# Kernel optimization log

Measured on AMD Instinct MI355X. Metric: run time of the kernel, lower is better.

Reference implementation:

```python
import jax, jax.numpy as jnp
import numpy as np

B, S, R, H = 16, 2048, 196, 768


def setup_inputs() -> dict:
    key = jax.random.key(0)
    ks = jax.random.split(key, 7)
    sc = 1.0 / np.sqrt(H)
    return {
        "text_features": jax.random.normal(ks[0], (B, S, H), jnp.float32),
        "img_features": jax.random.normal(ks[1], (B, R, H), jnp.float32),
        "W_text": jax.random.normal(ks[2], (H, H), jnp.float32) * sc,
        "b_text": jax.random.normal(ks[3], (H,), jnp.float32) * sc,
        "W_img": jax.random.normal(ks[4], (H, H), jnp.float32) * sc,
        "w_att": jax.random.normal(ks[5], (2 * H,), jnp.float32) * sc,
        "b_att": jax.random.normal(ks[6], (1,), jnp.float32) * sc,
    }


def reference(text_features, img_features, W_text, b_text, W_img, w_att, b_att):
    # Original: repeat text over regions, repeat img over seq, project, concat,
    # tanh, score via att_linear, softmax over regions, weighted sum of img.
    # tanh(concat(t, i)) = concat(tanh(t), tanh(i)), and the concat linear
    # splits into two dot products, so we avoid materializing (B,S,R,2H).
    H_ = text_features.shape[-1]
    t = jnp.tanh(jnp.einsum('bsh,oh->bso', text_features, W_text) + b_text)  # (B,S,H)
    i = jnp.tanh(jnp.einsum('brh,oh->bro', img_features, W_img))             # (B,R,H)
    w1, w2 = w_att[:H_], w_att[H_:]
    # score[b,s,r] = t[b,s]@w1 + i[b,r]@w2 + b_att
    scores = (t @ w1)[:, :, None] + (i @ w2)[:, None, :] + b_att[0]          # (B,S,R)
    att = jax.nn.softmax(scores, axis=-1)
    # weighted sum over regions of the ORIGINAL img features
    return jnp.einsum('bsr,brh->bsh', att, img_features)                      # (B,S,H)
```

## Files before the change

kernel.cpp:

```cpp
#include <hip/hip_runtime.h>
#include <math.h>

#define Bb   16
#define Ss   2048
#define Rr   196
#define Hh   768
#define Mtot (Bb * Rr)
#define NT   (Hh / 64)
#define LDA  72

typedef __attribute__((ext_vector_type(8))) short short8;
typedef __attribute__((ext_vector_type(4))) short short4v;
typedef __attribute__((ext_vector_type(4))) float f32x4;

__device__ inline short f2bf(float f) {
    unsigned u = __builtin_bit_cast(unsigned, f);
    u += 0x7fff + ((u >> 16) & 1);
    return (short)(u >> 16);
}

__global__ __launch_bounds__(256) void k0_cvt(
    const f32x4* __restrict__ a, short4v* __restrict__ da, int na4,
    const f32x4* __restrict__ b, short4v* __restrict__ db)
{
    int gid = blockIdx.x * 256 + threadIdx.x;
    const f32x4* s;
    short4v* d;
    int i;
    if (gid < na4) { s = a; d = da; i = gid; }
    else           { s = b; d = db; i = gid - na4; }
    f32x4 x = s[i];
    short4v o;
    o.x = f2bf(x.x); o.y = f2bf(x.y); o.z = f2bf(x.z); o.w = f2bf(x.w);
    d[i] = o;
}

template <bool FROM_F32>
__global__ __launch_bounds__(256) void k1_mfma(
    const void* __restrict__ Ap, const void* __restrict__ Bp,
    const float* __restrict__ w_att, float* __restrict__ part)
{
    const int m0   = blockIdx.x * 64;
    const int n0   = blockIdx.y * 64;
    const int t    = threadIdx.x;
    const int lane = t & 63;
    const int wv   = t >> 6;
    const int wm   = (wv & 1) * 32;
    const int wn   = (wv >> 1) * 32;
    const int col  = lane & 15;
    const int quad = lane >> 4;

    __shared__ short As[64 * LDA];
    __shared__ short Bs[64 * LDA];
    __shared__ float red[64][2];

    f32x4 acc[2][2] = {};

    const int sm = t >> 2;
    const int sq = t & 3;

    for (int k0 = 0; k0 < Hh; k0 += 64) {
        short8 areg[2], breg[2];
        if (FROM_F32) {
            const float* A = (const float*)Ap;
            const float* B = (const float*)Bp;
#pragma unroll
            for (int j = 0; j < 2; ++j) {
                float4 lo = *(const float4*)&A[(size_t)(m0 + sm) * Hh + k0 + sq * 16 + j * 8];
                float4 hi = *(const float4*)&A[(size_t)(m0 + sm) * Hh + k0 + sq * 16 + j * 8 + 4];
                areg[j][0] = f2bf(lo.x); areg[j][1] = f2bf(lo.y);
                areg[j][2] = f2bf(lo.z); areg[j][3] = f2bf(lo.w);
                areg[j][4] = f2bf(hi.x); areg[j][5] = f2bf(hi.y);
                areg[j][6] = f2bf(hi.z); areg[j][7] = f2bf(hi.w);
                lo = *(const float4*)&B[(size_t)(n0 + sm) * Hh + k0 + sq * 16 + j * 8];
                hi = *(const float4*)&B[(size_t)(n0 + sm) * Hh + k0 + sq * 16 + j * 8 + 4];
                breg[j][0] = f2bf(lo.x); breg[j][1] = f2bf(lo.y);
                breg[j][2] = f2bf(lo.z); breg[j][3] = f2bf(lo.w);
                breg[j][4] = f2bf(hi.x); breg[j][5] = f2bf(hi.y);
                breg[j][6] = f2bf(hi.z); breg[j][7] = f2bf(hi.w);
            }
        } else {
            const short* A = (const short*)Ap;
            const short* B = (const short*)Bp;
#pragma unroll
            for (int j = 0; j < 2; ++j) {
                areg[j] = *(const short8*)&A[(size_t)(m0 + sm) * Hh + k0 + sq * 16 + j * 8];
                breg[j] = *(const short8*)&B[(size_t)(n0 + sm) * Hh + k0 + sq * 16 + j * 8];
            }
        }
        __syncthreads();
#pragma unroll
        for (int j = 0; j < 2; ++j) {
            *(short8*)&As[sm * LDA + sq * 16 + j * 8] = areg[j];
            *(short8*)&Bs[sm * LDA + sq * 16 + j * 8] = breg[j];
        }
        __syncthreads();
#pragma unroll
        for (int kk = 0; kk < 64; kk += 32) {
            short8 a0 = *(const short8*)&As[(wm +      col) * LDA + kk + quad * 8];
            short8 a1 = *(const short8*)&As[(wm + 16 + col) * LDA + kk + quad * 8];
            short8 b0 = *(const short8*)&Bs[(wn +      col) * LDA + kk + quad * 8];
            short8 b1 = *(const short8*)&Bs[(wn + 16 + col) * LDA + kk + quad * 8];
            acc[0][0] = __builtin_amdgcn_mfma_f32_16x16x32_bf16(a0, b0, acc[0][0], 0, 0, 0);
            acc[0][1] = __builtin_amdgcn_mfma_f32_16x16x32_bf16(a0, b1, acc[0][1], 0, 0, 0);
            acc[1][0] = __builtin_amdgcn_mfma_f32_16x16x32_bf16(a1, b0, acc[1][0], 0, 0, 0);
            acc[1][1] = __builtin_amdgcn_mfma_f32_16x16x32_bf16(a1, b1, acc[1][1], 0, 0, 0);
        }
    }

    const float* w2 = w_att + Hh;
    float w2v0 = w2[n0 + wn + col];
    float w2v1 = w2[n0 + wn + 16 + col];

#pragma unroll
    for (int mi = 0; mi < 2; ++mi) {
#pragma unroll
        for (int r = 0; r < 4; ++r) {
            float s = tanhf(acc[mi][0][r]) * w2v0 + tanhf(acc[mi][1][r]) * w2v1;
            s += __shfl_xor(s, 1, 64);
            s += __shfl_xor(s, 2, 64);
            s += __shfl_xor(s, 4, 64);
            s += __shfl_xor(s, 8, 64);
            if (col == 0)
                red[wm + mi * 16 + quad * 4 + r][wn >> 5] = s;
        }
    }
    __syncthreads();
    if (t < 64)
        part[blockIdx.y * Mtot + m0 + t] = red[t][0] + red[t][1];
}

__global__ __launch_bounds__(256) void k2_softmax_v(
    const float* __restrict__ part,
    const float* __restrict__ img,
    float* __restrict__ v)
{
    const int b = blockIdx.x;
    const int t = threadIdx.x;

    __shared__ float p[Rr];
    __shared__ float redbuf[256];
    __shared__ float a2[4][65];

    float myv = -INFINITY;
    if (t < Rr) {
        float s = 0.f;
#pragma unroll
        for (int nt = 0; nt < NT; ++nt) s += part[nt * Mtot + b * Rr + t];
        p[t] = s;
        myv = s;
    }
    redbuf[t] = myv;
    __syncthreads();
    for (int off = 128; off > 0; off >>= 1) {
        if (t < off) redbuf[t] = fmaxf(redbuf[t], redbuf[t + off]);
        __syncthreads();
    }
    const float mx = redbuf[0];
    __syncthreads();

    float e = 0.f;
    if (t < Rr) e = expf(p[t] - mx);
    redbuf[t] = e;
    __syncthreads();
    for (int off = 128; off > 0; off >>= 1) {
        if (t < off) redbuf[t] += redbuf[t + off];
        __syncthreads();
    }
    const float inv = 1.f / redbuf[0];
    __syncthreads();
    if (t < Rr) p[t] = e * inv;
    __syncthreads();

    const int h  = blockIdx.y * 64 + (t & 63);
    const int rg = t >> 6;
    const float* imgb = img + (size_t)b * Rr * Hh + h;
    float s = 0.f;
#pragma unroll 7
    for (int r = rg * 49; r < rg * 49 + 49; ++r)
        s = fmaf(p[r], imgb[(size_t)r * Hh], s);
    a2[rg][t & 63] = s;
    __syncthreads();
    if (t < 64)
        v[b * Hh + blockIdx.y * 64 + t] = a2[0][t] + a2[1][t] + a2[2][t] + a2[3][t];
}

__global__ __launch_bounds__(256) void k3_bcast(
    const f32x4* __restrict__ v4,
    f32x4* __restrict__ out)
{
    const int gid   = blockIdx.x * 256 + threadIdx.x;
    const int per_b = Ss * (Hh / 4);
    const int b     = gid / per_b;
    const int h4    = gid % (Hh / 4);
    f32x4 val = v4[b * (Hh / 4) + h4];
    __builtin_nontemporal_store(val, &out[gid]);
}

extern "C" void kernel_launch(void* const* d_in, const int* in_sizes, int n_in,
                              void* d_out, int out_size, void* d_ws, size_t ws_size,
                              hipStream_t stream)
{
    const float* img   = (const float*)d_in[1];
    const float* W_img = (const float*)d_in[4];
    const float* w_att = (const float*)d_in[5];

    float* part = (float*)d_ws;
    float* v    = part + NT * Mtot;
    size_t off  = ((size_t)(NT * Mtot + Bb * Hh) * 4 + 15) & ~(size_t)15;
    short* imgbf = (short*)((char*)d_ws + off);
    short* Wbf   = imgbf + (size_t)Mtot * Hh;
    const size_t need = off + ((size_t)Mtot * Hh + (size_t)Hh * Hh) * 2;

    float* out = (float*)d_out;
    const bool usebf = (ws_size >= need);

    if (usebf) {
        const int na4 = (Mtot * Hh) / 4;
        const int nb4 = (Hh * Hh) / 4;
        k0_cvt<<<(na4 + nb4) / 256, 256, 0, stream>>>(
            (const f32x4*)img, (short4v*)imgbf, na4,
            (const f32x4*)W_img, (short4v*)Wbf);
        k1_mfma<false><<<dim3(Mtot / 64, NT), 256, 0, stream>>>(imgbf, Wbf, w_att, part);
    } else {
        k1_mfma<true><<<dim3(Mtot / 64, NT), 256, 0, stream>>>(img, W_img, w_att, part);
    }

    k2_softmax_v<<<dim3(Bb, NT), 256, 0, stream>>>(part, img, v);

    const int total4 = Bb * Ss * (Hh / 4);
    k3_bcast<<<total4 / 256, 256, 0, stream>>>((const f32x4*)v, (f32x4*)out);
}
```

Baseline: 198.5 us.

## Double-buffer bf16 GEMM via direct global-to-LDS loads with XOR swizzle; wave-shuffle softmax

The bf16 projection kernel now stages tiles with global_load_lds straight into a double-buffered, XOR-swizzled shared tile, so the next K tile loads while MFMAs run on the current one and the register round trip is skipped. The padded LDS layout is replaced by a swizzle to avoid bank conflicts. The softmax kernel swaps its shared-memory tree reductions for wave shuffles, which cuts the number of barriers. Overall time is likely dominated by the 200MB broadcast store, so these changes may have little visible effect.

```diff
diff --git a/kernel.cpp b/kernel.cpp
--- a/kernel.cpp
+++ b/kernel.cpp
@@ -17,6 +17,12 @@
     unsigned u = __builtin_bit_cast(unsigned, f);
     u += 0x7fff + ((u >> 16) & 1);
     return (short)(u >> 16);
+}
+
+__device__ __forceinline__ void gload_lds16(const void* g, void* l) {
+    __builtin_amdgcn_global_load_lds(
+        (const __attribute__((address_space(1))) void*)g,
+        (__attribute__((address_space(3))) void*)l, 16, 0, 0);
 }
 
 __global__ __launch_bounds__(256) void k0_cvt(
@@ -35,9 +41,8 @@
     d[i] = o;
 }
 
-template <bool FROM_F32>
-__global__ __launch_bounds__(256) void k1_mfma(
-    const void* __restrict__ Ap, const void* __restrict__ Bp,
+__global__ __launch_bounds__(256) void k1_mfma_bf16(
+    const short* __restrict__ A, const short* __restrict__ B,
     const float* __restrict__ w_att, float* __restrict__ part)
 {
     const int m0   = blockIdx.x * 64;
@@ -50,6 +55,95 @@
     const int col  = lane & 15;
     const int quad = lane >> 4;
 
+    __shared__ short As[2][64 * 64];
+    __shared__ short Bs[2][64 * 64];
+    __shared__ float red[64][2];
+
+    f32x4 acc[2][2] = {};
+
+    const int r0  = t >> 3;
+    const int glt = (t & 7) ^ (r0 & 7);
+    const short* srcA = A + (size_t)(m0 + r0) * Hh + glt * 8;
+    const short* srcB = B + (size_t)(n0 + r0) * Hh + glt * 8;
+    const int lo = wv * 512;
+
+    const auto stage = [&](int buf, int koff) {
+        gload_lds16(srcA + koff,           &As[buf][lo]);
+        gload_lds16(srcA + koff + 32 * Hh, &As[buf][lo + 2048]);
+        gload_lds16(srcB + koff,           &Bs[buf][lo]);
+        gload_lds16(srcB + koff + 32 * Hh, &Bs[buf][lo + 2048]);
+    };
+
+    const int rowA0 = (wm +      col) * 64;
+    const int rowA1 = (wm + 16 + col) * 64;
+    const int rowB0 = (wn +      col) * 64;
+    const int rowB1 = (wn + 16 + col) * 64;
+    const int ph0 = ((quad    ) ^ (col & 7)) * 8;
+    const int ph1 = ((quad + 4) ^ (col & 7)) * 8;
+
+    stage(0, 0);
+    __syncthreads();
+#pragma unroll
+    for (int kt = 0; kt < NT; ++kt) {
+        const int cur = kt & 1;
+        if (kt + 1 < NT) stage(cur ^ 1, (kt + 1) * 64);
+        const short* as = As[cur];
+        const short* bs = Bs[cur];
+        short8 a00 = *(const short8*)&as[rowA0 + ph0];
+        short8 a10 = *(const short8*)&as[rowA1 + ph0];
+        short8 b00 = *(const short8*)&bs[rowB0 + ph0];
+        short8 b10 = *(const short8*)&bs[rowB1 + ph0];
+        short8 a01 = *(const short8*)&as[rowA0 + ph1];
+        short8 a11 = *(const short8*)&as[rowA1 + ph1];
+        short8 b01 = *(const short8*)&bs[rowB0 + ph1];
+        short8 b11 = *(const short8*)&bs[rowB1 + ph1];
+        acc[0][0] = __builtin_amdgcn_mfma_f32_16x16x32_bf16(a00, b00, acc[0][0], 0, 0, 0);
+        acc[0][1] = __builtin_amdgcn_mfma_f32_16x16x32_bf16(a00, b10, acc[0][1], 0, 0, 0);
+        acc[1][0] = __builtin_amdgcn_mfma_f32_16x16x32_bf16(a10, b00, acc[1][0], 0, 0, 0);
+        acc[1][1] = __builtin_amdgcn_mfma_f32_16x16x32_bf16(a10, b10, acc[1][1], 0, 0, 0);
+        acc[0][0] = __builtin_amdgcn_mfma_f32_16x16x32_bf16(a01, b01, acc[0][0], 0, 0, 0);
+        acc[0][1] = __builtin_amdgcn_mfma_f32_16x16x32_bf16(a01, b11, acc[0][1], 0, 0, 0);
+        acc[1][0] = __builtin_amdgcn_mfma_f32_16x16x32_bf16(a11, b01, acc[1][0], 0, 0, 0);
+        acc[1][1] = __builtin_amdgcn_mfma_f32_16x16x32_bf16(a11, b11, acc[1][1], 0, 0, 0);
+        __syncthreads();
+    }
+
+    const float* w2 = w_att + Hh;
+    float w2v0 = w2[n0 + wn + col];
+    float w2v1 = w2[n0 + wn + 16 + col];
+
+#pragma unroll
+    for (int mi = 0; mi < 2; ++mi) {
+#pragma unroll
+        for (int r = 0; r < 4; ++r) {
+            float s = tanhf(acc[mi][0][r]) * w2v0 + tanhf(acc[mi][1][r]) * w2v1;
+            s += __shfl_xor(s, 1, 64);
+            s += __shfl_xor(s, 2, 64);
+            s += __shfl_xor(s, 4, 64);
+            s += __shfl_xor(s, 8, 64);
+            if (col == 0)
+                red[wm + mi * 16 + quad * 4 + r][wn >> 5] = s;
+        }
+    }
+    __syncthreads();
+    if (t < 64)
+        part[blockIdx.y * Mtot + m0 + t] = red[t][0] + red[t][1];
+}
+
+__global__ __launch_bounds__(256) void k1_mfma_f32(
+    const float* __restrict__ A, const float* __restrict__ B,
+    const float* __restrict__ w_att, float* __restrict__ part)
+{
+    const int m0   = blockIdx.x * 64;
+    const int n0   = blockIdx.y * 64;
+    const int t    = threadIdx.x;
+    const int lane = t & 63;
+    const int wv   = t >> 6;
+    const int wm   = (wv & 1) * 32;
+    const int wn   = (wv >> 1) * 32;
+    const int col  = lane & 15;
+    const int quad = lane >> 4;
+
     __shared__ short As[64 * LDA];
     __shared__ short Bs[64 * LDA];
     __shared__ float red[64][2];
@@ -61,32 +155,20 @@
 
     for (int k0 = 0; k0 < Hh; k0 += 64) {
         short8 areg[2], breg[2];
-        if (FROM_F32) {
-            const float* A = (const float*)Ap;
-            const float* B = (const float*)Bp;
-#pragma unroll
-            for (int j = 0; j < 2; ++j) {
-                float4 lo = *(const float4*)&A[(size_t)(m0 + sm) * Hh + k0 + sq * 16 + j * 8];
-                float4 hi = *(const float4*)&A[(size_t)(m0 + sm) * Hh + k0 + sq * 16 + j * 8 + 4];
-                areg[j][0] = f2bf(lo.x); areg[j][1] = f2bf(lo.y);
-                areg[j][2] = f2bf(lo.z); areg[j][3] = f2bf(lo.w);
-                areg[j][4] = f2bf(hi.x); areg[j][5] = f2bf(hi.y);
-                areg[j][6] = f2bf(hi.z); areg[j][7] = f2bf(hi.w);
-                lo = *(const float4*)&B[(size_t)(n0 + sm) * Hh + k0 + sq * 16 + j * 8];
-                hi = *(const float4*)&B[(size_t)(n0 + sm) * Hh + k0 + sq * 16 + j * 8 + 4];
-                breg[j][0] = f2bf(lo.x); breg[j][1] = f2bf(lo.y);
-                breg[j][2] = f2bf(lo.z); breg[j][3] = f2bf(lo.w);
-                breg[j][4] = f2bf(hi.x); breg[j][5] = f2bf(hi.y);
-                breg[j][6] = f2bf(hi.z); breg[j][7] = f2bf(hi.w);
-            }
-        } else {
-            const short* A = (const short*)Ap;
-            const short* B = (const short*)Bp;
-#pragma unroll
-            for (int j = 0; j < 2; ++j) {
-                areg[j] = *(const short8*)&A[(size_t)(m0 + sm) * Hh + k0 + sq * 16 + j * 8];
-                breg[j] = *(const short8*)&B[(size_t)(n0 + sm) * Hh + k0 + sq * 16 + j * 8];
-            }
+#pragma unroll
+        for (int j = 0; j < 2; ++j) {
+            float4 lo = *(const float4*)&A[(size_t)(m0 + sm) * Hh + k0 + sq * 16 + j * 8];
+            float4 hi = *(const float4*)&A[(size_t)(m0 + sm) * Hh + k0 + sq * 16 + j * 8 + 4];
+            areg[j][0] = f2bf(lo.x); areg[j][1] = f2bf(lo.y);
+            areg[j][2] = f2bf(lo.z); areg[j][3] = f2bf(lo.w);
+            areg[j][4] = f2bf(hi.x); areg[j][5] = f2bf(hi.y);
+            areg[j][6] = f2bf(hi.z); areg[j][7] = f2bf(hi.w);
+            lo = *(const float4*)&B[(size_t)(n0 + sm) * Hh + k0 + sq * 16 + j * 8];
+            hi = *(const float4*)&B[(size_t)(n0 + sm) * Hh + k0 + sq * 16 + j * 8 + 4];
+            breg[j][0] = f2bf(lo.x); breg[j][1] = f2bf(lo.y);
+            breg[j][2] = f2bf(lo.z); breg[j][3] = f2bf(lo.w);
+            breg[j][4] = f2bf(hi.x); breg[j][5] = f2bf(hi.y);
+            breg[j][6] = f2bf(hi.z); breg[j][7] = f2bf(hi.w);
         }
         __syncthreads();
 #pragma unroll
@@ -135,51 +217,47 @@
     const float* __restrict__ img,
     float* __restrict__ v)
 {
-    const int b = blockIdx.x;
-    const int t = threadIdx.x;
+    const int b    = blockIdx.x;
+    const int t    = threadIdx.x;
+    const int lane = t & 63;
+    const int wv   = t >> 6;
 
     __shared__ float p[Rr];
-    __shared__ float redbuf[256];
+    __shared__ float wred[4];
     __shared__ float a2[4][65];
 
-    float myv = -INFINITY;
+    float s = 0.f;
     if (t < Rr) {
-        float s = 0.f;
 #pragma unroll
         for (int nt = 0; nt < NT; ++nt) s += part[nt * Mtot + b * Rr + t];
-        p[t] = s;
-        myv = s;
-    }
-    redbuf[t] = myv;
-    __syncthreads();
-    for (int off = 128; off > 0; off >>= 1) {
-        if (t < off) redbuf[t] = fmaxf(redbuf[t], redbuf[t + off]);
-        __syncthreads();
-    }
-    const float mx = redbuf[0];
-    __syncthreads();
-
-    float e = 0.f;
-    if (t < Rr) e = expf(p[t] - mx);
-    redbuf[t] = e;
-    __syncthreads();
-    for (int off = 128; off > 0; off >>= 1) {
-        if (t < off) redbuf[t] += redbuf[t + off];
-        __syncthreads();
-    }
-    const float inv = 1.f / redbuf[0];
-    __syncthreads();
+    }
+
+    float m = (t < Rr) ? s : -INFINITY;
+#pragma unroll
+    for (int off = 1; off < 64; off <<= 1) m = fmaxf(m, __shfl_xor(m, off, 64));
+    if (lane == 0) wred[wv] = m;
+    __syncthreads();
+    const float mx = fmaxf(fmaxf(wred[0], wred[1]), fmaxf(wred[2], wred[3]));
+
+    float e = (t < Rr) ? expf(s - mx) : 0.f;
+    float sum = e;
+#pragma unroll
+    for (int off = 1; off < 64; off <<= 1) sum += __shfl_xor(sum, off, 64);
+    __syncthreads();
+    if (lane == 0) wred[wv] = sum;
+    __syncthreads();
+    const float inv = 1.f / (wred[0] + wred[1] + wred[2] + wred[3]);
     if (t < Rr) p[t] = e * inv;
     __syncthreads();
 
     const int h  = blockIdx.y * 64 + (t & 63);
     const int rg = t >> 6;
     const float* imgb = img + (size_t)b * Rr * Hh + h;
-    float s = 0.f;
+    float acc = 0.f;
 #pragma unroll 7
     for (int r = rg * 49; r < rg * 49 + 49; ++r)
-        s = fmaf(p[r], imgb[(size_t)r * Hh], s);
-    a2[rg][t & 63] = s;
+        acc = fmaf(p[r], imgb[(size_t)r * Hh], acc);
+    a2[rg][t & 63] = acc;
     __syncthreads();
     if (t < 64)
         v[b * Hh + blockIdx.y * 64 + t] = a2[0][t] + a2[1][t] + a2[2][t] + a2[3][t];
@@ -221,9 +299,9 @@
         k0_cvt<<<(na4 + nb4) / 256, 256, 0, stream>>>(
             (const f32x4*)img, (short4v*)imgbf, na4,
             (const f32x4*)W_img, (short4v*)Wbf);
-        k1_mfma<false><<<dim3(Mtot / 64, NT), 256, 0, stream>>>(imgbf, Wbf, w_att, part);
+        k1_mfma_bf16<<<dim3(Mtot / 64, NT), 256, 0, stream>>>(imgbf, Wbf, w_att, part);
     } else {
-        k1_mfma<true><<<dim3(Mtot / 64, NT), 256, 0, stream>>>(img, W_img, w_att, part);
+        k1_mfma_f32<<<dim3(Mtot / 64, NT), 256, 0, stream>>>(img, W_img, w_att, part);
     }
 
     k2_softmax_v<<<dim3(Bb, NT), 256, 0, stream>>>(part, img, v);
```

Measured after the change: 195.0 us. About the same (-1.7%).
